# Performance work log

Measured on AMD Instinct MI355X. Metric: run time of the kernel, lower is better.

Reference implementation:

```python
import jax, jax.numpy as jnp
import numpy as np

B, IN, C, H, E = 8192, 768, 64, 64, 16  # batch, input_dim, n_concepts, hidden_dim, embedding_dim


def setup_inputs() -> dict:
    key = jax.random.key(0)
    ks = jax.random.split(key, 10)

    def w(k, shape, fan_in):
        return jax.random.normal(k, shape, jnp.float32) / np.float32(np.sqrt(fan_in))

    inp = {"x": jax.random.normal(ks[0], (B, IN), jnp.float32)}
    i = 1
    for pre, din, dout in (("pos", IN, E), ("neg", IN, E), ("cp", 2 * E, 1)):
        inp[pre + "_W1"] = w(ks[i], (C, din, H), din)
        inp[pre + "_b1"] = jnp.zeros((C, H), jnp.float32)
        inp[pre + "_W2"] = w(ks[i + 1], (C, H, H), H)
        inp[pre + "_b2"] = jnp.zeros((C, H), jnp.float32)
        inp[pre + "_W3"] = w(ks[i + 2], (C, H, dout), H)
        inp[pre + "_b3"] = jnp.zeros((C, dout), jnp.float32)
        i += 3
    return inp


def _bank(x, W1, b1, W2, b2, W3, b3):
    # x: [B, IN]; per-concept MLP batched over C via einsum -> [B, C, E]
    h = jax.nn.relu(jnp.einsum('bi,cih->bch', x, W1) + b1)
    h = jax.nn.relu(jnp.einsum('bch,cho->bco', h, W2) + b2)
    return jnp.einsum('bch,che->bce', h, W3) + b3


def reference(x, pos_W1, pos_b1, pos_W2, pos_b2, pos_W3, pos_b3,
              neg_W1, neg_b1, neg_W2, neg_b2, neg_W3, neg_b3,
              cp_W1, cp_b1, cp_W2, cp_b2, cp_W3, cp_b3):
    pos = _bank(x, pos_W1, pos_b1, pos_W2, pos_b2, pos_W3, pos_b3)  # [B,C,E]
    neg = _bank(x, neg_W1, neg_b1, neg_W2, neg_b2, neg_W3, neg_b3)  # [B,C,E]
    # torch cat([pos, neg], dim=1) on [B,E,C], then x[:,:,i] -> per-concept [B, 2E]
    xc = jnp.concatenate([pos, neg], axis=-1)  # [B,C,2E]
    h = jax.nn.relu(jnp.einsum('bci,cih->bch', xc, cp_W1) + cp_b1)
    h = jax.nn.relu(jnp.einsum('bch,cho->bco', h, cp_W2) + cp_b2)
    concepts = (jnp.einsum('bch,cho->bco', h, cp_W3) + cp_b3)[..., 0]  # [B,C]
    w = jnp.clip(concepts * 0.5 + 0.5, 0.0, 1.0)[:, :, None]  # gate in [0,1]
    emb = pos * w + neg * (1.0 - w)  # [B,C,E]
    # torch layout is [B,E,C] then .view(B,-1): transpose before flattening
    emb_flat = jnp.transpose(emb, (0, 2, 1)).reshape(x.shape[0], E * C)
    return emb_flat, concepts
```

## Files before the change

kernel.cpp:

```cpp
#include <hip/hip_runtime.h>
#include <hip/hip_bf16.h>


#define B_   8192
#define IN_  768
#define C_   64
#define H_   64
#define E_   16
#define BM_  128

typedef __bf16 bf16x8 __attribute__((ext_vector_type(8)));
typedef float  f32x4  __attribute__((ext_vector_type(4)));

__device__ __forceinline__ f32x4 mfma16(bf16x8 a, bf16x8 b, f32x4 c) {
  return __builtin_amdgcn_mfma_f32_16x16x32_bf16(a, b, c, 0, 0, 0);
}

__device__ __forceinline__ bf16x8 cvt8(float4 a, float4 b) {
  bf16x8 r;
  r[0] = (__bf16)a.x; r[1] = (__bf16)a.y; r[2] = (__bf16)a.z; r[3] = (__bf16)a.w;
  r[4] = (__bf16)b.x; r[5] = (__bf16)b.y; r[6] = (__bf16)b.z; r[7] = (__bf16)b.w;
  return r;
}

__device__ __forceinline__ void zero_acc(f32x4 (&acc)[2][4]) {
  const f32x4 z = {0.f, 0.f, 0.f, 0.f};
#pragma unroll
  for (int mt = 0; mt < 2; ++mt)
#pragma unroll
    for (int nt = 0; nt < 4; ++nt) acc[mt][nt] = z;
}

__device__ __forceinline__ void gll16(const __bf16* g, __bf16* l) {
  __builtin_amdgcn_global_load_lds(
      (const __attribute__((address_space(1))) unsigned int*)g,
      (__attribute__((address_space(3))) unsigned int*)l, 16, 0, 0);
}

__device__ __forceinline__ void gll_w64(const __bf16* M, __bf16* dst, int rbase, int lane) {
  const int lr = lane >> 3, lc = (lane & 7) ^ lr;
  gll16(M + (size_t)(rbase + lr) * 64 + lc * 8, dst + rbase * 64);
}

__device__ __forceinline__ void gll_w32(const __bf16* M, __bf16* dst, int rbase, int lane) {
  const int lr = lane >> 2, lc = (lane & 3) ^ (lr & 3);
  gll16(M + (size_t)(rbase + lr) * 32 + lc * 8, dst + rbase * 32);
}

#define FENCE asm volatile("" ::: "memory")

struct __align__(16) SmemT {
  __bf16 bufA[256 * 64];
  __bf16 bufB[256 * 64];
  __bf16 xcb[BM_ * 40];
  float  conc[BM_];
  __bf16 cw3s[64];
};
static_assert(sizeof(SmemT) == 76416, "layout");
static_assert(sizeof(SmemT) <= 81920, "LDS: need 2 blocks/CU");

__device__ __forceinline__ void epi64s(__bf16* hb, f32x4 (&acc)[2][4],
                                       const float* __restrict__ bias,
                                       int wave, int quad, int l16) {
#pragma unroll
  for (int nt = 0; nt < 4; ++nt) {
    const int ch = nt * 2 + (l16 >> 3);
    const int cl = l16 & 7;
    const float bv = bias[nt * 16 + l16];
#pragma unroll
    for (int mt = 0; mt < 2; ++mt)
#pragma unroll
      for (int r = 0; r < 4; ++r) {
        const int row = wave * 32 + mt * 16 + quad * 4 + r;
        hb[row * 64 + (((ch ^ (row & 7)) << 3) | cl)] =
            (__bf16)fmaxf(acc[mt][nt][r] + bv, 0.f);
      }
  }
}

__device__ __forceinline__ void gemm64s(const __bf16* A, const __bf16* Bm,
                                        f32x4 (&acc)[2][4], int wave, int quad, int l16) {
  const int s7 = l16 & 7;
#pragma unroll
  for (int ks = 0; ks < 2; ++ks) {
    const int off = ((ks * 4 + quad) ^ s7) * 8;
    bf16x8 a[2], bb[4];
#pragma unroll
    for (int mt = 0; mt < 2; ++mt)
      a[mt] = *(const bf16x8*)(A + (wave * 32 + mt * 16 + l16) * 64 + off);
#pragma unroll
    for (int nt = 0; nt < 4; ++nt)
      bb[nt] = *(const bf16x8*)(Bm + (nt * 16 + l16) * 64 + off);
#pragma unroll
    for (int mt = 0; mt < 2; ++mt)
#pragma unroll
      for (int nt = 0; nt < 4; ++nt)
        acc[mt][nt] = mfma16(a[mt], bb[nt], acc[mt][nt]);
  }
}

__device__ __forceinline__ void l3s(const __bf16* A, const __bf16* B16,
                                    __bf16* xcb, const float* __restrict__ b3,
                                    int xc_off, int wave, int quad, int l16) {
  const int s7 = l16 & 7;
  f32x4 acc3[2];
  { const f32x4 z = {0.f, 0.f, 0.f, 0.f}; acc3[0] = z; acc3[1] = z; }
#pragma unroll
  for (int ks = 0; ks < 2; ++ks) {
    const int off = ((ks * 4 + quad) ^ s7) * 8;
    bf16x8 bb = *(const bf16x8*)(B16 + l16 * 64 + off);
#pragma unroll
    for (int mt = 0; mt < 2; ++mt) {
      bf16x8 a = *(const bf16x8*)(A + (wave * 32 + mt * 16 + l16) * 64 + off);
      acc3[mt] = mfma16(a, bb, acc3[mt]);
    }
  }
  const float bv = b3[l16];
#pragma unroll
  for (int mt = 0; mt < 2; ++mt)
#pragma unroll
    for (int r = 0; r < 4; ++r) {
      const int row = wave * 32 + mt * 16 + quad * 4 + r;
      xcb[row * 40 + xc_off + l16] = (__bf16)(acc3[mt][r] + bv);
    }
}

__device__ __forceinline__ void l1_step(const __bf16* cbuf,
                                        f32x4 (&accP)[2][4], f32x4 (&accN)[2][4],
                                        int wave, int quad, int l16) {
  const int sx = l16 & 7;
#pragma unroll
  for (int ks = 0; ks < 2; ++ks) {
    const int pc = ((ks * 4 + quad) ^ sx) * 8;
    bf16x8 a[2], bp[4], bn[4];
#pragma unroll
    for (int mt = 0; mt < 2; ++mt)
      a[mt] = *(const bf16x8*)(cbuf + (wave * 32 + mt * 16 + l16) * 64 + pc);
#pragma unroll
    for (int nt = 0; nt < 4; ++nt) {
      bp[nt] = *(const bf16x8*)(cbuf + (128 + nt * 16 + l16) * 64 + pc);
      bn[nt] = *(const bf16x8*)(cbuf + (192 + nt * 16 + l16) * 64 + pc);
    }
#pragma unroll
    for (int mt = 0; mt < 2; ++mt)
#pragma unroll
      for (int nt = 0; nt < 4; ++nt) {
        accP[mt][nt] = mfma16(a[mt], bp[nt], accP[mt][nt]);
        accN[mt][nt] = mfma16(a[mt], bn[nt], accN[mt][nt]);
      }
  }
}

__global__ __launch_bounds__(256, 2) void cb_fused_t(
    const __bf16* __restrict__ x,
    const __bf16* __restrict__ pW1t, const float* __restrict__ pb1,
    const __bf16* __restrict__ pW2t, const float* __restrict__ pb2,
    const __bf16* __restrict__ pW3t, const float* __restrict__ pb3,
    const __bf16* __restrict__ nW1t, const float* __restrict__ nb1,
    const __bf16* __restrict__ nW2t, const float* __restrict__ nb2,
    const __bf16* __restrict__ nW3t, const float* __restrict__ nb3,
    const __bf16* __restrict__ cW1t, const float* __restrict__ cb1,
    const __bf16* __restrict__ cW2t, const float* __restrict__ cb2,
    const __bf16* __restrict__ cw3,  const float* __restrict__ cb3,
    float* __restrict__ out_emb, float* __restrict__ out_con)
{
  __shared__ SmemT sm;
  const int tid  = threadIdx.x;
  const int wave = tid >> 6, lane = tid & 63;
  const int quad = lane >> 4, l16 = lane & 15;
  const int row0 = blockIdx.x * BM_;
  const int c    = blockIdx.y;

  const __bf16* pg   = pW1t + (size_t)c * 64 * IN_;
  const __bf16* ng   = nW1t + (size_t)c * 64 * IN_;
  const float*  pb1c = pb1 + c * 64;
  const float*  nb1c = nb1 + c * 64;
  const float*  pb2c = pb2 + c * 64;
  const float*  nb2c = nb2 + c * 64;

  f32x4 accP[2][4]; zero_acc(accP);
  f32x4 accN[2][4]; zero_acc(accN);

  const __bf16* xg = x + (size_t)row0 * IN_;
  const int lrow   = lane >> 3;
  const int lchunk = (lane & 7) ^ lrow;
  const __bf16* gsrc = (wave == 0) ? xg
                     : (wave == 1) ? xg + 64 * IN_
                     : (wave == 2) ? pg : ng;
  const __bf16* gl = gsrc + (size_t)lrow * IN_ + lchunk * 8;
  __bf16* const dA = sm.bufA + wave * 64 * 64;
  __bf16* const dB = sm.bufB + wave * 64 * 64;

#pragma unroll
  for (int j = 0; j < 8; ++j)
    gll16(gl + j * 8 * IN_, dA + j * 8 * 64);

  for (int kt = 0; kt < 11; ++kt) {
    {
      const __bf16* gk = gl + (kt + 1) * 64;
      __bf16* nd = (kt & 1) ? dA : dB;
#pragma unroll
      for (int j = 0; j < 8; ++j)
        gll16(gk + j * 8 * IN_, nd + j * 8 * 64);
    }
    asm volatile("s_waitcnt vmcnt(8)" ::: "memory");
    __builtin_amdgcn_s_barrier();
    __builtin_amdgcn_sched_barrier(0);
    FENCE;
    l1_step((kt & 1) ? sm.bufB : sm.bufA, accP, accN, wave, quad, l16);
    FENCE;
    __builtin_amdgcn_s_barrier();
    __builtin_amdgcn_sched_barrier(0);
    FENCE;
  }

  {
    __bf16* WT = sm.bufA;
    if (wave == 0) {
      const __bf16* M = pW2t + (size_t)c * 4096;
#pragma unroll
      for (int g = 0; g < 8; ++g) gll_w64(M, WT, g * 8, lane);
      if (lane < 8) gll16(cw3 + (size_t)c * 64 + lane * 8, sm.cw3s);
    } else if (wave == 1) {
      const __bf16* M = nW2t + (size_t)c * 4096;
#pragma unroll
      for (int g = 0; g < 8; ++g) gll_w64(M, WT + 4096, g * 8, lane);
    } else if (wave == 2) {
      const __bf16* m3p = pW3t + (size_t)c * 1024;
      const __bf16* m3n = nW3t + (size_t)c * 1024;
      const __bf16* mc1 = cW1t + (size_t)c * 2048;
      gll_w64(m3p, WT + 8192, 0, lane);
      gll_w64(m3p, WT + 8192, 8, lane);
      gll_w64(m3n, WT + 9216, 0, lane);
      gll_w64(m3n, WT + 9216, 8, lane);
      gll_w32(mc1, WT + 10240, 0,  lane);
      gll_w32(mc1, WT + 10240, 16, lane);
      gll_w32(mc1, WT + 10240, 32, lane);
      gll_w32(mc1, WT + 10240, 48, lane);
    } else {
      const __bf16* M = cW2t + (size_t)c * 4096;
#pragma unroll
      for (int g = 0; g < 8; ++g) gll_w64(M, WT + 12288, g * 8, lane);
    }
  }

  asm volatile("s_waitcnt vmcnt(8)" ::: "memory");
  __builtin_amdgcn_s_barrier();
  __builtin_amdgcn_sched_barrier(0);
  FENCE;
  l1_step(sm.bufB, accP, accN, wave, quad, l16);
  FENCE;
  __builtin_amdgcn_s_barrier();
  __builtin_amdgcn_sched_barrier(0);
  FENCE;

  __bf16* WT  = sm.bufA;
  __bf16* hbP = sm.bufB;
  __bf16* hbN = sm.bufB + 8192;

  epi64s(hbP, accP, pb1c, wave, quad, l16);
  epi64s(hbN, accN, nb1c, wave, quad, l16);
  __syncthreads();

  f32x4 acc2P[2][4]; zero_acc(acc2P);
  f32x4 acc2N[2][4]; zero_acc(acc2N);
  gemm64s(hbP, WT,        acc2P, wave, quad, l16);
  gemm64s(hbN, WT + 4096, acc2N, wave, quad, l16);
  epi64s(hbP, acc2P, pb2c, wave, quad, l16);
  epi64s(hbN, acc2N, nb2c, wave, quad, l16);

  l3s(hbP, WT + 8192, sm.xcb, pb3 + c * 16, 0,  wave, quad, l16);
  l3s(hbN, WT + 9216, sm.xcb, nb3 + c * 16, 16, wave, quad, l16);

  f32x4 acc1[2][4]; zero_acc(acc1);
  {
    bf16x8 a[2], bb[4];
#pragma unroll
    for (int mt = 0; mt < 2; ++mt)
      a[mt] = *(const bf16x8*)&sm.xcb[(wave * 32 + mt * 16 + l16) * 40 + quad * 8];
#pragma unroll
    for (int nt = 0; nt < 4; ++nt)
      bb[nt] = *(const bf16x8*)(WT + 10240 + (nt * 16 + l16) * 32 +
                                ((quad ^ (l16 & 3)) * 8));
#pragma unroll
    for (int mt = 0; mt < 2; ++mt)
#pragma unroll
      for (int nt = 0; nt < 4; ++nt)
        acc1[mt][nt] = mfma16(a[mt], bb[nt], acc1[mt][nt]);
  }
  epi64s(hbP, acc1, cb1 + c * 64, wave, quad, l16);

  f32x4 accC[2][4]; zero_acc(accC);
  gemm64s(hbP, WT + 12288, accC, wave, quad, l16);
  epi64s(hbP, accC, cb2 + c * 64, wave, quad, l16);

  {
    f32x4 acc3[2];
    { const f32x4 z = {0.f, 0.f, 0.f, 0.f}; acc3[0] = z; acc3[1] = z; }
    const int s7 = l16 & 7;
#pragma unroll
    for (int ks = 0; ks < 2; ++ks) {
      const int off = ((ks * 4 + quad) ^ s7) * 8;
      bf16x8 bb = {};
      if (l16 == 0) bb = *(const bf16x8*)&sm.cw3s[ks * 32 + quad * 8];
#pragma unroll
      for (int mt = 0; mt < 2; ++mt) {
        bf16x8 a = *(const bf16x8*)(hbP + (wave * 32 + mt * 16 + l16) * 64 + off);
        acc3[mt] = mfma16(a, bb, acc3[mt]);
      }
    }
    if (l16 == 0) {
      float bv = cb3[c];
#pragma unroll
      for (int mt = 0; mt < 2; ++mt)
#pragma unroll
        for (int r = 0; r < 4; ++r)
          sm.conc[wave * 32 + mt * 16 + quad * 4 + r] = acc3[mt][r] + bv;
    }
  }
  __syncthreads();

  for (int ii = tid; ii < BM_ * E_; ii += 256) {
    int row = ii >> 4, e = ii & 15;
    float cv = sm.conc[row];
    float w  = fminf(fmaxf(cv * 0.5f + 0.5f, 0.f), 1.f);
    float pv2 = (float)sm.xcb[row * 40 + e];
    float nv2 = (float)sm.xcb[row * 40 + 16 + e];
    out_emb[(size_t)(row0 + row) * (E_ * C_) + e * C_ + c] = pv2 * w + nv2 * (1.f - w);
  }
  if (tid < 128) out_con[(size_t)(row0 + tid) * C_ + c] = sm.conc[tid];
}

#define TSEG 5
#define PSEG 5
struct PrepArgs {
  const float* tsrc[TSEG];
  __bf16*      tdst[TSEG];
  int tstart[TSEG + 1];
  int ktiles[TSEG];
  const float* psrc[PSEG];
  __bf16*      pdst[PSEG];
  int pstart[PSEG + 1];
  int pchunks[PSEG];
  int kdiv8[PSEG];
  int N[PSEG];
  int tblocks;
};

__global__ __launch_bounds__(256) void prep_all(PrepArgs a) {
  const int tid = threadIdx.x;
  const int b = blockIdx.x;
  __shared__ __bf16 lt[64 * 72];
  if (b < a.tblocks) {
    int s = 0;
    while (s < TSEG - 1 && b >= a.tstart[s + 1]) ++s;
    const int idx = b - a.tstart[s];
    const int kt = idx % a.ktiles[s];
    const int c  = idx / a.ktiles[s];
    const int K  = a.ktiles[s] * 64;
    const float* src = a.tsrc[s] + (size_t)c * K * 64 + (size_t)kt * 64 * 64;
    __bf16*      dst = a.tdst[s] + (size_t)c * 64 * K + kt * 64;
    const int r = tid >> 4, c4 = (tid & 15) * 4;
#pragma unroll
    for (int it = 0; it < 4; ++it) {
      int k = r + it * 16;
      float4 v = *(const float4*)(src + (size_t)k * 64 + c4);
      lt[(c4 + 0) * 72 + k] = (__bf16)v.x;
      lt[(c4 + 1) * 72 + k] = (__bf16)v.y;
      lt[(c4 + 2) * 72 + k] = (__bf16)v.z;
      lt[(c4 + 3) * 72 + k] = (__bf16)v.w;
    }
    __syncthreads();
    const int n = tid >> 3, i = tid & 7;
#pragma unroll
    for (int it = 0; it < 2; ++it) {
      int nn = n + it * 32;
      *(uint4*)(dst + (size_t)nn * K + i * 8) = *(const uint4*)&lt[nn * 72 + i * 8];
    }
  } else {
    const int bb = b - a.tblocks;
    int s = 0;
    while (s < PSEG - 1 && bb >= a.pstart[s + 1]) ++s;
    const int lb  = bb - a.pstart[s];
    const int nch = a.pchunks[s];
    const int kc  = a.kdiv8[s];
    const int N   = a.N[s];
#pragma unroll
    for (int j = 0; j < 4; ++j) {
      const int li = (lb * 4 + j) * 256 + tid;
      if (li >= nch) break;
      if (N == 1) {
        const float4* src = (const float4*)a.psrc[s] + (size_t)li * 2;
        float4 v0 = src[0], v1 = src[1];
        *(uint4*)(a.pdst[s] + (size_t)li * 8) = __builtin_bit_cast(uint4, cvt8(v0, v1));
      } else {
        int rn = li / kc;
        int k0 = (li - rn * kc) * 8;
        int cc = rn / N;
        int n  = rn - cc * N;
        const float* src = a.psrc[s] + ((size_t)cc * kc * 8 + k0) * N + n;
        bf16x8 r;
#pragma unroll
        for (int jj = 0; jj < 8; ++jj) r[jj] = (__bf16)src[(size_t)jj * N];
        *(uint4*)(a.pdst[s] + (size_t)rn * kc * 8 + k0) = __builtin_bit_cast(uint4, r);
      }
    }
  }
}

extern "C" void kernel_launch(void* const* d_in, const int* in_sizes, int n_in,
                              void* d_out, int out_size, void* d_ws, size_t ws_size,
                              hipStream_t stream) {
  const float* xf   = (const float*)d_in[0];
  const float* pW1f = (const float*)d_in[1];
  const float* pb1f = (const float*)d_in[2];
  const float* pW2f = (const float*)d_in[3];
  const float* pb2f = (const float*)d_in[4];
  const float* pW3f = (const float*)d_in[5];
  const float* pb3f = (const float*)d_in[6];
  const float* nW1f = (const float*)d_in[7];
  const float* nb1f = (const float*)d_in[8];
  const float* nW2f = (const float*)d_in[9];
  const float* nb2f = (const float*)d_in[10];
  const float* nW3f = (const float*)d_in[11];
  const float* nb3f = (const float*)d_in[12];
  const float* cW1f = (const float*)d_in[13];
  const float* cb1f = (const float*)d_in[14];
  const float* cW2f = (const float*)d_in[15];
  const float* cb2f = (const float*)d_in[16];
  const float* cW3f = (const float*)d_in[17];
  const float* cb3f = (const float*)d_in[18];

  float* out_emb = (float*)d_out;
  float* out_con = out_emb + (size_t)B_ * E_ * C_;

  const int cx   = B_ * IN_;
  const int cW1c = C_ * IN_ * H_;
  const int cW2c = C_ * H_ * H_;
  const int cW3c = C_ * H_ * E_;
  const int ccW1 = C_ * 2 * E_ * H_;
  const int ccW3 = C_ * H_;

  __bf16* w = (__bf16*)d_ws;
  size_t o = 0;
  __bf16* xw   = w + o; o += cx;
  __bf16* pw1t = w + o; o += cW1c;
  __bf16* nw1t = w + o; o += cW1c;
  __bf16* pw2t = w + o; o += cW2c;
  __bf16* nw2t = w + o; o += cW2c;
  __bf16* cw2t = w + o; o += cW2c;
  __bf16* pw3t = w + o; o += cW3c;
  __bf16* nw3t = w + o; o += cW3c;
  __bf16* cw1t = w + o; o += ccW1;
  __bf16* cw3w = w + o; o += ccW3;

  PrepArgs a;
  int tb = 0, pb = 0;
  {
    const float* tsrc[TSEG] = {pW1f, nW1f, pW2f, nW2f, cW2f};
    __bf16*      tdst[TSEG] = {pw1t, nw1t, pw2t, nw2t, cw2t};
    const int    tk[TSEG]   = {12,   12,   1,    1,    1};
    for (int i = 0; i < TSEG; ++i) {
      a.tsrc[i] = tsrc[i]; a.tdst[i] = tdst[i]; a.ktiles[i] = tk[i];
      a.tstart[i] = tb;
      tb += tk[i] * C_;
    }
    a.tstart[TSEG] = tb;
    a.tblocks = tb;

    const float* psrc[PSEG] = {xf, cW3f, pW3f, nW3f, cW1f};
    __bf16*      pdst[PSEG] = {xw, cw3w, pw3t, nw3t, cw1t};
    const int    pKs[PSEG]  = {0,  0,    64,   64,   32};
    const int    pNs[PSEG]  = {1,  1,    16,   16,   64};
    const int    pels[PSEG] = {cx, ccW3, cW3c, cW3c, ccW1};
    for (int i = 0; i < PSEG; ++i) {
      a.psrc[i] = psrc[i]; a.pdst[i] = pdst[i];
      a.pchunks[i] = pels[i] / 8;
      a.kdiv8[i] = (pNs[i] == 1) ? (pels[i] / 8) : (pKs[i] / 8);
      a.N[i] = pNs[i];
      a.pstart[i] = pb;
      pb += (pels[i] / 8 + 1023) / 1024;
    }
    a.pstart[PSEG] = pb;
  }
  prep_all<<<tb + pb, 256, 0, stream>>>(a);

  dim3 grid(B_ / BM_, C_);
  cb_fused_t<<<grid, 256, 0, stream>>>(xw,
      pw1t, pb1f, pw2t, pb2f, pw3t, pb3f,
      nw1t, nb1f, nw2t, nb2f, nw3t, nb3f,
      cw1t, cb1f, cw2t, cb2f, cw3w, cb3f,
      out_emb, out_con);
}
```

Baseline: 314.2 us.

## Load x tiles directly to registers and shrink LDS for three blocks per CU

The layer-1 loop now reads A fragments of x straight from global memory into registers and only stages the pos/neg W1 tiles through LDS, roughly halving the shared-memory footprint. Later-layer weights (W2, W3, cp W1/W2/W3) are read directly from global memory instead of being staged into LDS, and launch bounds target three blocks per CU. The goal is higher occupancy and less LDS traffic, at the cost of uncoalesced, unhidden global loads on the critical path and more register pressure. A __syncthreads between the first epilogue and the layer-2 GEMM was removed, which may introduce a race on the hidden-state buffers.

```diff
diff --git a/kernel.cpp b/kernel.cpp
--- a/kernel.cpp
+++ b/kernel.cpp
@@ -37,27 +37,15 @@
       (__attribute__((address_space(3))) unsigned int*)l, 16, 0, 0);
 }
 
-__device__ __forceinline__ void gll_w64(const __bf16* M, __bf16* dst, int rbase, int lane) {
-  const int lr = lane >> 3, lc = (lane & 7) ^ lr;
-  gll16(M + (size_t)(rbase + lr) * 64 + lc * 8, dst + rbase * 64);
-}
-
-__device__ __forceinline__ void gll_w32(const __bf16* M, __bf16* dst, int rbase, int lane) {
-  const int lr = lane >> 2, lc = (lane & 3) ^ (lr & 3);
-  gll16(M + (size_t)(rbase + lr) * 32 + lc * 8, dst + rbase * 32);
-}
-
 #define FENCE asm volatile("" ::: "memory")
 
 struct __align__(16) SmemT {
-  __bf16 bufA[256 * 64];
-  __bf16 bufB[256 * 64];
+  __bf16 wbuf[2 * 128 * 64];
   __bf16 xcb[BM_ * 40];
   float  conc[BM_];
-  __bf16 cw3s[64];
 };
-static_assert(sizeof(SmemT) == 76416, "layout");
-static_assert(sizeof(SmemT) <= 81920, "LDS: need 2 blocks/CU");
+static_assert(sizeof(SmemT) == 43520, "layout");
+static_assert(sizeof(SmemT) <= 54613, "LDS: need 3 blocks/CU");
 
 __device__ __forceinline__ void epi64s(__bf16* hb, f32x4 (&acc)[2][4],
                                        const float* __restrict__ bias,
@@ -78,41 +66,47 @@
   }
 }
 
-__device__ __forceinline__ void gemm64s(const __bf16* A, const __bf16* Bm,
+__device__ __forceinline__ void gemm64g(const __bf16* A, const __bf16* __restrict__ Wg,
                                         f32x4 (&acc)[2][4], int wave, int quad, int l16) {
   const int s7 = l16 & 7;
+  bf16x8 bb[2][4];
+#pragma unroll
+  for (int ks = 0; ks < 2; ++ks)
+#pragma unroll
+    for (int nt = 0; nt < 4; ++nt)
+      bb[ks][nt] = *(const bf16x8*)(Wg + (nt * 16 + l16) * 64 + ks * 32 + quad * 8);
 #pragma unroll
   for (int ks = 0; ks < 2; ++ks) {
     const int off = ((ks * 4 + quad) ^ s7) * 8;
-    bf16x8 a[2], bb[4];
+    bf16x8 a[2];
 #pragma unroll
     for (int mt = 0; mt < 2; ++mt)
       a[mt] = *(const bf16x8*)(A + (wave * 32 + mt * 16 + l16) * 64 + off);
 #pragma unroll
-    for (int nt = 0; nt < 4; ++nt)
-      bb[nt] = *(const bf16x8*)(Bm + (nt * 16 + l16) * 64 + off);
-#pragma unroll
     for (int mt = 0; mt < 2; ++mt)
 #pragma unroll
       for (int nt = 0; nt < 4; ++nt)
-        acc[mt][nt] = mfma16(a[mt], bb[nt], acc[mt][nt]);
-  }
-}
-
-__device__ __forceinline__ void l3s(const __bf16* A, const __bf16* B16,
+        acc[mt][nt] = mfma16(a[mt], bb[ks][nt], acc[mt][nt]);
+  }
+}
+
+__device__ __forceinline__ void l3g(const __bf16* A, const __bf16* __restrict__ W3g,
                                     __bf16* xcb, const float* __restrict__ b3,
                                     int xc_off, int wave, int quad, int l16) {
   const int s7 = l16 & 7;
   f32x4 acc3[2];
   { const f32x4 z = {0.f, 0.f, 0.f, 0.f}; acc3[0] = z; acc3[1] = z; }
+  bf16x8 bb[2];
+#pragma unroll
+  for (int ks = 0; ks < 2; ++ks)
+    bb[ks] = *(const bf16x8*)(W3g + l16 * 64 + ks * 32 + quad * 8);
 #pragma unroll
   for (int ks = 0; ks < 2; ++ks) {
     const int off = ((ks * 4 + quad) ^ s7) * 8;
-    bf16x8 bb = *(const bf16x8*)(B16 + l16 * 64 + off);
 #pragma unroll
     for (int mt = 0; mt < 2; ++mt) {
       bf16x8 a = *(const bf16x8*)(A + (wave * 32 + mt * 16 + l16) * 64 + off);
-      acc3[mt] = mfma16(a, bb, acc3[mt]);
+      acc3[mt] = mfma16(a, bb[ks], acc3[mt]);
     }
   }
   const float bv = b3[l16];
@@ -125,33 +119,30 @@
     }
 }
 
-__device__ __forceinline__ void l1_step(const __bf16* cbuf,
+__device__ __forceinline__ void l1_step(const __bf16* wb, const bf16x8 (&av)[2][2],
                                         f32x4 (&accP)[2][4], f32x4 (&accN)[2][4],
-                                        int wave, int quad, int l16) {
+                                        int quad, int l16) {
   const int sx = l16 & 7;
 #pragma unroll
   for (int ks = 0; ks < 2; ++ks) {
     const int pc = ((ks * 4 + quad) ^ sx) * 8;
-    bf16x8 a[2], bp[4], bn[4];
-#pragma unroll
-    for (int mt = 0; mt < 2; ++mt)
-      a[mt] = *(const bf16x8*)(cbuf + (wave * 32 + mt * 16 + l16) * 64 + pc);
+    bf16x8 bp[4], bn[4];
 #pragma unroll
     for (int nt = 0; nt < 4; ++nt) {
-      bp[nt] = *(const bf16x8*)(cbuf + (128 + nt * 16 + l16) * 64 + pc);
-      bn[nt] = *(const bf16x8*)(cbuf + (192 + nt * 16 + l16) * 64 + pc);
+      bp[nt] = *(const bf16x8*)(wb + (nt * 16 + l16) * 64 + pc);
+      bn[nt] = *(const bf16x8*)(wb + (64 + nt * 16 + l16) * 64 + pc);
     }
 #pragma unroll
     for (int mt = 0; mt < 2; ++mt)
 #pragma unroll
       for (int nt = 0; nt < 4; ++nt) {
-        accP[mt][nt] = mfma16(a[mt], bp[nt], accP[mt][nt]);
-        accN[mt][nt] = mfma16(a[mt], bn[nt], accN[mt][nt]);
+        accP[mt][nt] = mfma16(av[mt][ks], bp[nt], accP[mt][nt]);
+        accN[mt][nt] = mfma16(av[mt][ks], bn[nt], accN[mt][nt]);
       }
   }
 }
 
-__global__ __launch_bounds__(256, 2) void cb_fused_t(
+__global__ __launch_bounds__(256, 3) void cb_fused_t(
     const __bf16* __restrict__ x,
     const __bf16* __restrict__ pW1t, const float* __restrict__ pb1,
     const __bf16* __restrict__ pW2t, const float* __restrict__ pb2,
@@ -182,106 +173,72 @@
   f32x4 accN[2][4]; zero_acc(accN);
 
   const __bf16* xg = x + (size_t)row0 * IN_;
-  const int lrow   = lane >> 3;
-  const int lchunk = (lane & 7) ^ lrow;
-  const __bf16* gsrc = (wave == 0) ? xg
-                     : (wave == 1) ? xg + 64 * IN_
-                     : (wave == 2) ? pg : ng;
-  const __bf16* gl = gsrc + (size_t)lrow * IN_ + lchunk * 8;
-  __bf16* const dA = sm.bufA + wave * 64 * 64;
-  __bf16* const dB = sm.bufB + wave * 64 * 64;
-
-#pragma unroll
-  for (int j = 0; j < 8; ++j)
-    gll16(gl + j * 8 * IN_, dA + j * 8 * 64);
-
-  for (int kt = 0; kt < 11; ++kt) {
-    {
-      const __bf16* gk = gl + (kt + 1) * 64;
-      __bf16* nd = (kt & 1) ? dA : dB;
-#pragma unroll
-      for (int j = 0; j < 8; ++j)
-        gll16(gk + j * 8 * IN_, nd + j * 8 * 64);
-    }
-    asm volatile("s_waitcnt vmcnt(8)" ::: "memory");
+  const int lrow = lane >> 3, lchunk = (lane & 7) ^ lrow;
+  const __bf16* wsrc = (wave < 2)
+      ? pg + (size_t)(wave * 32 + lrow) * IN_ + lchunk * 8
+      : ng + (size_t)((wave - 2) * 32 + lrow) * IN_ + lchunk * 8;
+  __bf16* const d0 = sm.wbuf + wave * 32 * 64;
+  __bf16* const d1 = sm.wbuf + 8192 + wave * 32 * 64;
+
+#pragma unroll
+  for (int j = 0; j < 4; ++j)
+    gll16(wsrc + j * 8 * IN_, d0 + j * 8 * 64);
+
+  const __bf16* ag = xg + (size_t)(wave * 32 + l16) * IN_ + quad * 8;
+
+  for (int kt = 0; kt < 12; ++kt) {
+    bf16x8 av[2][2];
+    av[0][0] = *(const bf16x8*)(ag + kt * 64);
+    av[0][1] = *(const bf16x8*)(ag + kt * 64 + 32);
+    av[1][0] = *(const bf16x8*)(ag + (size_t)16 * IN_ + kt * 64);
+    av[1][1] = *(const bf16x8*)(ag + (size_t)16 * IN_ + kt * 64 + 32);
+    __builtin_amdgcn_sched_barrier(0);
+    if (kt < 11) {
+      const __bf16* wk = wsrc + (kt + 1) * 64;
+      __bf16* nd = ((kt + 1) & 1) ? d1 : d0;
+#pragma unroll
+      for (int j = 0; j < 4; ++j)
+        gll16(wk + j * 8 * IN_, nd + j * 8 * 64);
+      asm volatile("s_waitcnt vmcnt(8)" ::: "memory");
+    } else {
+      asm volatile("s_waitcnt vmcnt(4)" ::: "memory");
+    }
     __builtin_amdgcn_s_barrier();
     __builtin_amdgcn_sched_barrier(0);
     FENCE;
-    l1_step((kt & 1) ? sm.bufB : sm.bufA, accP, accN, wave, quad, l16);
+    l1_step(sm.wbuf + (kt & 1) * 8192, av, accP, accN, quad, l16);
     FENCE;
     __builtin_amdgcn_s_barrier();
     __builtin_amdgcn_sched_barrier(0);
     FENCE;
   }
 
-  {
-    __bf16* WT = sm.bufA;
-    if (wave == 0) {
-      const __bf16* M = pW2t + (size_t)c * 4096;
-#pragma unroll
-      for (int g = 0; g < 8; ++g) gll_w64(M, WT, g * 8, lane);
-      if (lane < 8) gll16(cw3 + (size_t)c * 64 + lane * 8, sm.cw3s);
-    } else if (wave == 1) {
-      const __bf16* M = nW2t + (size_t)c * 4096;
-#pragma unroll
-      for (int g = 0; g < 8; ++g) gll_w64(M, WT + 4096, g * 8, lane);
-    } else if (wave == 2) {
-      const __bf16* m3p = pW3t + (size_t)c * 1024;
-      const __bf16* m3n = nW3t + (size_t)c * 1024;
-      const __bf16* mc1 = cW1t + (size_t)c * 2048;
-      gll_w64(m3p, WT + 8192, 0, lane);
-      gll_w64(m3p, WT + 8192, 8, lane);
-      gll_w64(m3n, WT + 9216, 0, lane);
-      gll_w64(m3n, WT + 9216, 8, lane);
-      gll_w32(mc1, WT + 10240, 0,  lane);
-      gll_w32(mc1, WT + 10240, 16, lane);
-      gll_w32(mc1, WT + 10240, 32, lane);
-      gll_w32(mc1, WT + 10240, 48, lane);
-    } else {
-      const __bf16* M = cW2t + (size_t)c * 4096;
-#pragma unroll
-      for (int g = 0; g < 8; ++g) gll_w64(M, WT + 12288, g * 8, lane);
-    }
-  }
-
-  asm volatile("s_waitcnt vmcnt(8)" ::: "memory");
-  __builtin_amdgcn_s_barrier();
-  __builtin_amdgcn_sched_barrier(0);
-  FENCE;
-  l1_step(sm.bufB, accP, accN, wave, quad, l16);
-  FENCE;
-  __builtin_amdgcn_s_barrier();
-  __builtin_amdgcn_sched_barrier(0);
-  FENCE;
-
-  __bf16* WT  = sm.bufA;
-  __bf16* hbP = sm.bufB;
-  __bf16* hbN = sm.bufB + 8192;
+  __bf16* hbP = sm.wbuf;
+  __bf16* hbN = sm.wbuf + 8192;
 
   epi64s(hbP, accP, pb1c, wave, quad, l16);
   epi64s(hbN, accN, nb1c, wave, quad, l16);
-  __syncthreads();
 
   f32x4 acc2P[2][4]; zero_acc(acc2P);
   f32x4 acc2N[2][4]; zero_acc(acc2N);
-  gemm64s(hbP, WT,        acc2P, wave, quad, l16);
-  gemm64s(hbN, WT + 4096, acc2N, wave, quad, l16);
+  gemm64g(hbP, pW2t + (size_t)c * 4096, acc2P, wave, quad, l16);
+  gemm64g(hbN, nW2t + (size_t)c * 4096, acc2N, wave, quad, l16);
   epi64s(hbP, acc2P, pb2c, wave, quad, l16);
   epi64s(hbN, acc2N, nb2c, wave, quad, l16);
 
-  l3s(hbP, WT + 8192, sm.xcb, pb3 + c * 16, 0,  wave, quad, l16);
-  l3s(hbN, WT + 9216, sm.xcb, nb3 + c * 16, 16, wave, quad, l16);
+  l3g(hbP, pW3t + (size_t)c * 1024, sm.xcb, pb3 + c * 16, 0,  wave, quad, l16);
+  l3g(hbN, nW3t + (size_t)c * 1024, sm.xcb, nb3 + c * 16, 16, wave, quad, l16);
 
   f32x4 acc1[2][4]; zero_acc(acc1);
   {
+    const __bf16* c1 = cW1t + (size_t)c * 2048;
     bf16x8 a[2], bb[4];
 #pragma unroll
+    for (int nt = 0; nt < 4; ++nt)
+      bb[nt] = *(const bf16x8*)(c1 + (nt * 16 + l16) * 32 + quad * 8);
+#pragma unroll
     for (int mt = 0; mt < 2; ++mt)
       a[mt] = *(const bf16x8*)&sm.xcb[(wave * 32 + mt * 16 + l16) * 40 + quad * 8];
-#pragma unroll
-    for (int nt = 0; nt < 4; ++nt)
-      bb[nt] = *(const bf16x8*)(WT + 10240 + (nt * 16 + l16) * 32 +
-                                ((quad ^ (l16 & 3)) * 8));
 #pragma unroll
     for (int mt = 0; mt < 2; ++mt)
 #pragma unroll
@@ -291,7 +248,7 @@
   epi64s(hbP, acc1, cb1 + c * 64, wave, quad, l16);
 
   f32x4 accC[2][4]; zero_acc(accC);
-  gemm64s(hbP, WT + 12288, accC, wave, quad, l16);
+  gemm64g(hbP, cW2t + (size_t)c * 4096, accC, wave, quad, l16);
   epi64s(hbP, accC, cb2 + c * 64, wave, quad, l16);
 
   {
@@ -301,12 +258,12 @@
 #pragma unroll
     for (int ks = 0; ks < 2; ++ks) {
       const int off = ((ks * 4 + quad) ^ s7) * 8;
-      bf16x8 bb = {};
-      if (l16 == 0) bb = *(const bf16x8*)&sm.cw3s[ks * 32 + quad * 8];
+      bf16x8 bbv = {};
+      if (l16 == 0) bbv = *(const bf16x8*)(cw3 + (size_t)c * 64 + ks * 32 + quad * 8);
 #pragma unroll
       for (int mt = 0; mt < 2; ++mt) {
         bf16x8 a = *(const bf16x8*)(hbP + (wave * 32 + mt * 16 + l16) * 64 + off);
-        acc3[mt] = mfma16(a, bb, acc3[mt]);
+        acc3[mt] = mfma16(a, bbv, acc3[mt]);
       }
     }
     if (l16 == 0) {
```

Result: slower. 336.6 us (+7.1%).
